# Kernel tuning notes

Hardware: AMD Instinct MI355X
Metric: run time of the kernel (lower is better)

The kernel has to match this reference:

```python
import jax, jax.numpy as jnp
import numpy as np

B, L, D, NID = 256, 512, 64, 10000


def _count_appearances(src_ids, dst_ids):
    # Equivalent to per-sample unique+bincount: for each position i,
    # count occurrences of that id in the src sequence and in the dst sequence.
    # src_ids, dst_ids: (B, L) int64. Padding id == 0 is masked to 0 afterward.
    src_in_src = (src_ids[:, :, None] == src_ids[:, None, :]).sum(-1)  # (B, L)
    src_in_dst = (src_ids[:, :, None] == dst_ids[:, None, :]).sum(-1)
    dst_in_src = (dst_ids[:, :, None] == src_ids[:, None, :]).sum(-1)
    dst_in_dst = (dst_ids[:, :, None] == dst_ids[:, None, :]).sum(-1)
    src_app = jnp.stack([src_in_src, src_in_dst], axis=-1).astype(jnp.float32)  # (B, L, 2)
    dst_app = jnp.stack([dst_in_src, dst_in_dst], axis=-1).astype(jnp.float32)
    src_app = jnp.where((src_ids == 0)[..., None], 0.0, src_app)
    dst_app = jnp.where((dst_ids == 0)[..., None], 0.0, dst_app)
    return src_app, dst_app


def _encode(app, W1, b1, W2, b2):
    # app: (B, L, 2) -> unsqueeze(-1) -> Linear(1->D) -> ReLU -> Linear(D->D) -> sum over channel dim 2
    h = jax.nn.relu(app[..., None] * W1[:, 0] + b1)          # (B, L, 2, D)
    out = jnp.einsum('blcd,ed->blce', h, W2) + b2             # (B, L, 2, D)
    return out.sum(axis=2)                                    # (B, L, D)


def setup_inputs() -> dict:
    key = jax.random.key(0)
    k1, k2, k3, k4, k5, k6 = jax.random.split(key, 6)
    return {
        'src_ids': jax.random.randint(k1, (B, L), 0, NID, dtype=jnp.int64) if jax.config.read('jax_enable_x64') else jax.random.randint(k1, (B, L), 0, NID).astype(jnp.int32),
        'dst_ids': jax.random.randint(k2, (B, L), 0, NID).astype(jnp.int32),
        'W1': jax.random.normal(k3, (D, 1), dtype=jnp.float32) * 0.5,
        'b1': jax.random.normal(k4, (D,), dtype=jnp.float32) * 0.1,
        'W2': jax.random.normal(k5, (D, D), dtype=jnp.float32) * (1.0 / np.sqrt(D)),
        'b2': jax.random.normal(k6, (D,), dtype=jnp.float32) * 0.1,
    }


def reference(src_ids, dst_ids, W1, b1, W2, b2):
    src_app, dst_app = _count_appearances(src_ids, dst_ids)
    src_feat = _encode(src_app, W1, b1, W2, b2)
    dst_feat = _encode(dst_app, W1, b1, W2, b2)
    return src_feat, dst_feat
```

## Files before the change

kernel.cpp:

```cpp
#include <hip/hip_runtime.h>

#define BB  256
#define LL  512
#define DD  64
#define NID 10000
#define NW  (NID / 2)

__global__ void build_table(const float* __restrict__ W1, const float* __restrict__ b1,
                            const float* __restrict__ W2, const float* __restrict__ b2,
                            float* __restrict__ T) {
    int a = blockIdx.x;
    int e = threadIdx.x;
    __shared__ float h[DD];
    h[e] = fmaxf((float)a * W1[e] + b1[e], 0.0f);
    __syncthreads();
    const float* w2row = W2 + e * DD;
    float acc = b2[e];
#pragma unroll
    for (int d = 0; d < DD; ++d) acc += h[d] * w2row[d];
    T[a * DD + e] = acc;
}

__global__ __launch_bounds__(512) void count_encode(
    const int* __restrict__ src_ids, const int* __restrict__ dst_ids,
    const float* __restrict__ T, float* __restrict__ out)
{
    __shared__ unsigned int hs[NW];
    __shared__ unsigned int hd[NW];
    __shared__ int sids[LL];
    __shared__ int dids[LL];
    __shared__ unsigned short as0[LL], as1[LL], ad0[LL], ad1[LL];

    const int t = threadIdx.x;
    const int b = blockIdx.x;

    for (int i = t; i < NW; i += 512) { hs[i] = 0u; hd[i] = 0u; }
    sids[t] = src_ids[b * LL + t];
    dids[t] = dst_ids[b * LL + t];
    __syncthreads();

    const int sid = sids[t];
    const int did = dids[t];
    atomicAdd(&hs[sid >> 1], 1u << ((sid & 1) * 16));
    atomicAdd(&hd[did >> 1], 1u << ((did & 1) * 16));
    __syncthreads();

    unsigned int c_ss = (hs[sid >> 1] >> ((sid & 1) * 16)) & 0xFFFFu;
    unsigned int c_sd = (hd[sid >> 1] >> ((sid & 1) * 16)) & 0xFFFFu;
    unsigned int c_ds = (hs[did >> 1] >> ((did & 1) * 16)) & 0xFFFFu;
    unsigned int c_dd = (hd[did >> 1] >> ((did & 1) * 16)) & 0xFFFFu;
    if (sid == 0) { c_ss = 0u; c_sd = 0u; }
    if (did == 0) { c_ds = 0u; c_dd = 0u; }
    as0[t] = (unsigned short)c_ss;
    as1[t] = (unsigned short)c_sd;
    ad0[t] = (unsigned short)c_ds;
    ad1[t] = (unsigned short)c_dd;
    __syncthreads();

    const float4* T4      = (const float4*)T;
    float4* out_src = (float4*)(out + (size_t)b * LL * DD);
    float4* out_dst = (float4*)(out + (size_t)BB * LL * DD + (size_t)b * LL * DD);
    const int q     = t & 15;
    const int lbase = t >> 4;

#pragma unroll 4
    for (int pass = 0; pass < 16; ++pass) {
        const int l = pass * 32 + lbase;
        const float4 s0 = T4[(int)as0[l] * 16 + q];
        const float4 s1 = T4[(int)as1[l] * 16 + q];
        float4 v;
        v.x = s0.x + s1.x; v.y = s0.y + s1.y; v.z = s0.z + s1.z; v.w = s0.w + s1.w;
        out_src[l * 16 + q] = v;
        const float4 d0 = T4[(int)ad0[l] * 16 + q];
        const float4 d1 = T4[(int)ad1[l] * 16 + q];
        float4 w;
        w.x = d0.x + d1.x; w.y = d0.y + d1.y; w.z = d0.z + d1.z; w.w = d0.w + d1.w;
        out_dst[l * 16 + q] = w;
    }
}

extern "C" void kernel_launch(void* const* d_in, const int* in_sizes, int n_in,
                              void* d_out, int out_size, void* d_ws, size_t ws_size,
                              hipStream_t stream) {
    const int*   src_ids = (const int*)d_in[0];
    const int*   dst_ids = (const int*)d_in[1];
    const float* W1      = (const float*)d_in[2];
    const float* b1      = (const float*)d_in[3];
    const float* W2      = (const float*)d_in[4];
    const float* b2      = (const float*)d_in[5];
    float* out = (float*)d_out;
    float* T   = (float*)d_ws;

    build_table<<<dim3(LL + 1), dim3(DD), 0, stream>>>(W1, b1, W2, b2, T);
    count_encode<<<dim3(BB), dim3(512), 0, stream>>>(src_ids, dst_ids, T, out);
}
```

Before: 90.86 us.

## Split counting and output streaming into separate kernels with grid-stride writer

Counting now writes packed per-row count pairs to a workspace buffer. A separate grid-stride kernel with many blocks streams the 64 MB output by gathering table rows, instead of 256 blocks each writing their own slice. The table build also caches W2 in shared memory and computes four rows per block, and the LDS histogram zeroing now uses uint4 stores. The aim is more parallelism and memory-level concurrency for the output write. The cost is an extra kernel launch and a round trip of the count buffer through global memory.

```diff
diff --git a/kernel.cpp b/kernel.cpp
--- a/kernel.cpp
+++ b/kernel.cpp
@@ -5,42 +5,50 @@
 #define DD  64
 #define NID 10000
 #define NW  (NID / 2)
+#define NROWS (2 * BB * LL)
+#define NT4  (NROWS * 16)
 
-__global__ void build_table(const float* __restrict__ W1, const float* __restrict__ b1,
-                            const float* __restrict__ W2, const float* __restrict__ b2,
-                            float* __restrict__ T) {
-    int a = blockIdx.x;
-    int e = threadIdx.x;
-    __shared__ float h[DD];
-    h[e] = fmaxf((float)a * W1[e] + b1[e], 0.0f);
+__global__ __launch_bounds__(256) void build_table(
+    const float* __restrict__ W1, const float* __restrict__ b1,
+    const float* __restrict__ W2, const float* __restrict__ b2,
+    float* __restrict__ T)
+{
+    __shared__ float w2l[DD][DD + 1];
+    __shared__ float hsh[4][DD];
+    const int t = threadIdx.x;
+    const int w = t >> 6;
+    const int e = t & 63;
+    for (int i = t; i < DD * DD; i += 256)
+        w2l[i >> 6][i & 63] = W2[i];
+    const int a = blockIdx.x * 4 + w;
+    hsh[w][e] = fmaxf((float)a * W1[e] + b1[e], 0.0f);
     __syncthreads();
-    const float* w2row = W2 + e * DD;
-    float acc = b2[e];
+    if (a <= LL) {
+        float acc = b2[e];
 #pragma unroll
-    for (int d = 0; d < DD; ++d) acc += h[d] * w2row[d];
-    T[a * DD + e] = acc;
+        for (int d = 0; d < DD; ++d)
+            acc = fmaf(hsh[w][d], w2l[e][d], acc);
+        T[a * DD + e] = acc;
+    }
 }
 
-__global__ __launch_bounds__(512) void count_encode(
+__global__ __launch_bounds__(512) void count_rows(
     const int* __restrict__ src_ids, const int* __restrict__ dst_ids,
-    const float* __restrict__ T, float* __restrict__ out)
+    unsigned int* __restrict__ R)
 {
     __shared__ unsigned int hs[NW];
     __shared__ unsigned int hd[NW];
-    __shared__ int sids[LL];
-    __shared__ int dids[LL];
-    __shared__ unsigned short as0[LL], as1[LL], ad0[LL], ad1[LL];
-
     const int t = threadIdx.x;
     const int b = blockIdx.x;
 
-    for (int i = t; i < NW; i += 512) { hs[i] = 0u; hd[i] = 0u; }
-    sids[t] = src_ids[b * LL + t];
-    dids[t] = dst_ids[b * LL + t];
+    uint4* z1 = (uint4*)hs;
+    uint4* z2 = (uint4*)hd;
+    const uint4 z = make_uint4(0u, 0u, 0u, 0u);
+    for (int i = t; i < NW / 4; i += 512) { z1[i] = z; z2[i] = z; }
+    const int sid = src_ids[b * LL + t];
+    const int did = dst_ids[b * LL + t];
     __syncthreads();
 
-    const int sid = sids[t];
-    const int did = dids[t];
     atomicAdd(&hs[sid >> 1], 1u << ((sid & 1) * 16));
     atomicAdd(&hd[did >> 1], 1u << ((did & 1) * 16));
     __syncthreads();
@@ -51,31 +59,25 @@
     unsigned int c_dd = (hd[did >> 1] >> ((did & 1) * 16)) & 0xFFFFu;
     if (sid == 0) { c_ss = 0u; c_sd = 0u; }
     if (did == 0) { c_ds = 0u; c_dd = 0u; }
-    as0[t] = (unsigned short)c_ss;
-    as1[t] = (unsigned short)c_sd;
-    ad0[t] = (unsigned short)c_ds;
-    ad1[t] = (unsigned short)c_dd;
-    __syncthreads();
+    R[b * LL + t]           = c_ss | (c_sd << 16);
+    R[BB * LL + b * LL + t] = c_ds | (c_dd << 16);
+}
 
-    const float4* T4      = (const float4*)T;
-    float4* out_src = (float4*)(out + (size_t)b * LL * DD);
-    float4* out_dst = (float4*)(out + (size_t)BB * LL * DD + (size_t)b * LL * DD);
-    const int q     = t & 15;
-    const int lbase = t >> 4;
-
-#pragma unroll 4
-    for (int pass = 0; pass < 16; ++pass) {
-        const int l = pass * 32 + lbase;
-        const float4 s0 = T4[(int)as0[l] * 16 + q];
-        const float4 s1 = T4[(int)as1[l] * 16 + q];
+__global__ __launch_bounds__(256) void stream_out(
+    const unsigned int* __restrict__ R, const float* __restrict__ T,
+    float4* __restrict__ out4)
+{
+    const float4* T4 = (const float4*)T;
+    int g = blockIdx.x * 256 + threadIdx.x;
+    const int stride = gridDim.x * 256;
+    for (; g < NT4; g += stride) {
+        const unsigned int r = R[g >> 4];
+        const int q = g & 15;
+        const float4 x = T4[(r & 0xFFFFu) * 16 + q];
+        const float4 y = T4[(r >> 16) * 16 + q];
         float4 v;
-        v.x = s0.x + s1.x; v.y = s0.y + s1.y; v.z = s0.z + s1.z; v.w = s0.w + s1.w;
-        out_src[l * 16 + q] = v;
-        const float4 d0 = T4[(int)ad0[l] * 16 + q];
-        const float4 d1 = T4[(int)ad1[l] * 16 + q];
-        float4 w;
-        w.x = d0.x + d1.x; w.y = d0.y + d1.y; w.z = d0.z + d1.z; w.w = d0.w + d1.w;
-        out_dst[l * 16 + q] = w;
+        v.x = x.x + y.x; v.y = x.y + y.y; v.z = x.z + y.z; v.w = x.w + y.w;
+        out4[g] = v;
     }
 }
 
@@ -88,9 +90,11 @@
     const float* b1      = (const float*)d_in[3];
     const float* W2      = (const float*)d_in[4];
     const float* b2      = (const float*)d_in[5];
-    float* out = (float*)d_out;
-    float* T   = (float*)d_ws;
 
-    build_table<<<dim3(LL + 1), dim3(DD), 0, stream>>>(W1, b1, W2, b2, T);
-    count_encode<<<dim3(BB), dim3(512), 0, stream>>>(src_ids, dst_ids, T, out);
+    float*        T = (float*)d_ws;
+    unsigned int* R = (unsigned int*)((char*)d_ws + (256 << 10));
+
+    build_table<<<dim3(129), dim3(256), 0, stream>>>(W1, b1, W2, b2, T);
+    count_rows<<<dim3(BB), dim3(512), 0, stream>>>(src_ids, dst_ids, R);
+    stream_out<<<dim3(2048), dim3(256), 0, stream>>>(R, T, (float4*)d_out);
 }
```

Result: slower. 94.19 us (+3.7%).
